# Optimization experiments

Hardware: AMD Instinct MI355X
Metric: run time of the kernel (lower is better)

The kernel has to match this reference:

```python
import jax, jax.numpy as jnp
import numpy as np

PAD_ID = 12975
HEADS = 16


def _sinusoid_table(n_position, d_hid):
    # pos / 10000^(2*(j//2)/d_hid), sin on even dims, cos on odd dims
    pos = jnp.arange(n_position, dtype=jnp.float32)[:, None]          # [P,1]
    j = jnp.arange(d_hid)
    angle = pos / jnp.power(10000.0, (2.0 * (j // 2) / d_hid).astype(jnp.float32))  # [P,D]
    table = jnp.where((j % 2) == 0, jnp.sin(angle), jnp.cos(angle))
    return table  # [P, D]


def setup_inputs() -> dict:
    key = jax.random.key(0)
    k1, k2 = jax.random.split(key)
    x = jax.random.randint(k1, (256, 200), 0, 32000, dtype=jnp.int64)
    weight = jax.random.normal(k2, (32000, 1024), dtype=jnp.float32) * 0.02
    return {"x": x, "weight": weight}


def reference(x, weight):
    B, S = x.shape
    D = weight.shape[1]

    # --- mask build (faithful to the python-loop semantics) ---
    m = x == PAD_ID                                   # [B,S]
    has_pad = jnp.any(m, axis=1)                      # [B]
    first = jnp.argmax(m, axis=1)                     # first True index (0 if none)
    # torch loop: if no True found, i ends at S-1 and idx[S-1:] is still set True
    first = jnp.where(has_pad, first, S - 1)          # [B]
    row_ge = jnp.arange(S)[None, :] >= first[:, None]  # [B,S] rows >= first are all-True
    remask = m[:, None, :] | row_ge[:, :, None]       # [B,S,S]
    mask = jnp.broadcast_to(remask[:, None, :, :], (B, HEADS, S, S))  # [B,H,S,S]

    # --- embedding + sinusoidal positional encoding (dropout in eval = identity) ---
    emb = weight[x]                                   # [B,S,D]
    pos_table = _sinusoid_table(S, D)                 # [S,D]
    out = emb + pos_table[None, :, :]                 # [B,S,D]
    return (out, mask)
```

## Files before the change

kernel.cpp:

```cpp
#include <hip/hip_runtime.h>
#include <math.h>

#define PAD_ID 12975
#define BB 256
#define SS 200
#define DD 1024
#define HH 16

#define WS_FIRST_BYTES 1024
#define WS_POST_BYTES  (SS * DD * 4)

__global__ void first_kernel(const int* __restrict__ x, int* __restrict__ first) {
    __shared__ int sfirst;
    const int b = blockIdx.x;
    if (threadIdx.x == 0) sfirst = SS - 1;
    __syncthreads();
    const int s = threadIdx.x;
    if (s < SS) {
        if (x[b * SS + s] == PAD_ID) atomicMin(&sfirst, s);
    }
    __syncthreads();
    if (threadIdx.x == 0) first[b] = sfirst;
}

__global__ void postable_kernel(float* __restrict__ posT) {
    const int idx = blockIdx.x * blockDim.x + threadIdx.x;
    if (idx >= SS * DD) return;
    const int s = idx >> 10;
    const int j = idx & (DD - 1);
    const int p = j >> 1;
    const float C = (float)(13.287712379549449 / 512.0);
    const float denom = exp2f((float)p * C);
    const float angle = (float)s / denom;
    posT[idx] = (j & 1) ? cosf(angle) : sinf(angle);
}

__global__ void mask_kernel(const int* __restrict__ x, const int* __restrict__ first,
                            float* __restrict__ mask) {
    const int total = BB * HH * SS * (SS / 4);
    const int stride = gridDim.x * blockDim.x;
    for (int c = blockIdx.x * blockDim.x + threadIdx.x; c < total; c += stride) {
        const int row = c / 50;
        const int j4  = c - row * 50;
        const int b   = row / (HH * SS);
        const int i   = row % SS;
        float4 v;
        if (i >= first[b]) {
            v = make_float4(1.f, 1.f, 1.f, 1.f);
        } else {
            const int4 xv = ((const int4*)x)[b * 50 + j4];
            v.x = (xv.x == PAD_ID) ? 1.f : 0.f;
            v.y = (xv.y == PAD_ID) ? 1.f : 0.f;
            v.z = (xv.z == PAD_ID) ? 1.f : 0.f;
            v.w = (xv.w == PAD_ID) ? 1.f : 0.f;
        }
        ((float4*)mask)[c] = v;
    }
}

__global__ void out_kernel(const int* __restrict__ x, const float* __restrict__ weight,
                           const float* __restrict__ posT, float* __restrict__ out) {
    const int row = blockIdx.x;
    const int s = row % SS;
    const int idx = x[row];
    const int t = threadIdx.x;
    const float4 w  = ((const float4*)(weight + (size_t)idx * DD))[t];
    const float4 pe = ((const float4*)(posT + (size_t)s * DD))[t];
    ((float4*)(out + (size_t)row * DD))[t] =
        make_float4(w.x + pe.x, w.y + pe.y, w.z + pe.z, w.w + pe.w);
}

__global__ void out_kernel_inline(const int* __restrict__ x, const float* __restrict__ weight,
                                  float* __restrict__ out) {
    const int row = blockIdx.x;
    const int s = row % SS;
    const int idx = x[row];
    const int t = threadIdx.x;
    const float C = (float)(13.287712379549449 / 512.0);
    const float p0 = (float)(2 * t);
    const float p1 = (float)(2 * t + 1);
    const float a0 = (float)s / exp2f(p0 * C);
    const float a1 = (float)s / exp2f(p1 * C);
    const float4 pe = make_float4(sinf(a0), cosf(a0), sinf(a1), cosf(a1));
    const float4 w = ((const float4*)(weight + (size_t)idx * DD))[t];
    ((float4*)(out + (size_t)row * DD))[t] =
        make_float4(w.x + pe.x, w.y + pe.y, w.z + pe.z, w.w + pe.w);
}

extern "C" void kernel_launch(void* const* d_in, const int* in_sizes, int n_in,
                              void* d_out, int out_size, void* d_ws, size_t ws_size,
                              hipStream_t stream) {
    const int*   x      = (const int*)d_in[0];
    const float* weight = (const float*)d_in[1];
    float* out  = (float*)d_out;
    float* mask = out + (size_t)BB * SS * DD;

    int*   first = (int*)d_ws;
    float* posT  = (float*)((char*)d_ws + WS_FIRST_BYTES);
    const bool useTable = ws_size >= (size_t)(WS_FIRST_BYTES + WS_POST_BYTES);

    first_kernel<<<BB, 256, 0, stream>>>(x, first);
    if (useTable) {
        postable_kernel<<<(SS * DD + 255) / 256, 256, 0, stream>>>(posT);
    }
    mask_kernel<<<8192, 256, 0, stream>>>(x, first, mask);
    if (useTable) {
        out_kernel<<<BB * SS, 256, 0, stream>>>(x, weight, posT, out);
    } else {
        out_kernel_inline<<<BB * SS, 256, 0, stream>>>(x, weight, out);
    }
}
```

Baseline: 193.3 us.

## Fuse prep and mask/output kernels into two launches with nontemporal stores

Merges the first-pad and positional-table kernels into one prep kernel, and runs the mask write and embedding+PE output in a single persistent kernel whose blocks are statically split between the two tasks. Both large write streams now use nontemporal stores. The aim is to cut launch overhead and let the two bandwidth-bound streams overlap. It drops the fallback for a small workspace, and the fixed block split may leave one half of the work finishing later than the other.

```diff
diff --git a/kernel.cpp b/kernel.cpp
--- a/kernel.cpp
+++ b/kernel.cpp
@@ -7,84 +7,75 @@
 #define DD 1024
 #define HH 16
 
+#define MASK_CHUNKS (BB * HH * SS * (SS / 4))
+#define OUT_ROWS    (BB * SS)
+
+#define NBLK 2048
+#define MBLK 1376
+
+typedef float f32x4 __attribute__((ext_vector_type(4)));
+typedef int   i32x4 __attribute__((ext_vector_type(4)));
+
 #define WS_FIRST_BYTES 1024
 #define WS_POST_BYTES  (SS * DD * 4)
 
-__global__ void first_kernel(const int* __restrict__ x, int* __restrict__ first) {
-    __shared__ int sfirst;
-    const int b = blockIdx.x;
-    if (threadIdx.x == 0) sfirst = SS - 1;
-    __syncthreads();
-    const int s = threadIdx.x;
-    if (s < SS) {
-        if (x[b * SS + s] == PAD_ID) atomicMin(&sfirst, s);
+__global__ void prep_kernel(const int* __restrict__ x, int* __restrict__ first,
+                            float* __restrict__ posT) {
+    const int idx = blockIdx.x * blockDim.x + threadIdx.x;
+    if (idx < SS * DD) {
+        const int s = idx >> 10;
+        const int j = idx & (DD - 1);
+        const int p = j >> 1;
+        const float C = (float)(13.287712379549449 / 512.0);
+        const float angle = (float)s / exp2f((float)p * C);
+        posT[idx] = (j & 1) ? cosf(angle) : sinf(angle);
     }
-    __syncthreads();
-    if (threadIdx.x == 0) first[b] = sfirst;
-}
-
-__global__ void postable_kernel(float* __restrict__ posT) {
-    const int idx = blockIdx.x * blockDim.x + threadIdx.x;
-    if (idx >= SS * DD) return;
-    const int s = idx >> 10;
-    const int j = idx & (DD - 1);
-    const int p = j >> 1;
-    const float C = (float)(13.287712379549449 / 512.0);
-    const float denom = exp2f((float)p * C);
-    const float angle = (float)s / denom;
-    posT[idx] = (j & 1) ? cosf(angle) : sinf(angle);
-}
-
-__global__ void mask_kernel(const int* __restrict__ x, const int* __restrict__ first,
-                            float* __restrict__ mask) {
-    const int total = BB * HH * SS * (SS / 4);
-    const int stride = gridDim.x * blockDim.x;
-    for (int c = blockIdx.x * blockDim.x + threadIdx.x; c < total; c += stride) {
-        const int row = c / 50;
-        const int j4  = c - row * 50;
-        const int b   = row / (HH * SS);
-        const int i   = row % SS;
-        float4 v;
-        if (i >= first[b]) {
-            v = make_float4(1.f, 1.f, 1.f, 1.f);
-        } else {
-            const int4 xv = ((const int4*)x)[b * 50 + j4];
-            v.x = (xv.x == PAD_ID) ? 1.f : 0.f;
-            v.y = (xv.y == PAD_ID) ? 1.f : 0.f;
-            v.z = (xv.z == PAD_ID) ? 1.f : 0.f;
-            v.w = (xv.w == PAD_ID) ? 1.f : 0.f;
-        }
-        ((float4*)mask)[c] = v;
+    if (blockIdx.x < BB) {
+        __shared__ int sfirst;
+        if (threadIdx.x == 0) sfirst = SS - 1;
+        __syncthreads();
+        if (threadIdx.x < SS && x[blockIdx.x * SS + threadIdx.x] == PAD_ID)
+            atomicMin(&sfirst, threadIdx.x);
+        __syncthreads();
+        if (threadIdx.x == 0) first[blockIdx.x] = sfirst;
     }
 }
 
-__global__ void out_kernel(const int* __restrict__ x, const float* __restrict__ weight,
-                           const float* __restrict__ posT, float* __restrict__ out) {
-    const int row = blockIdx.x;
-    const int s = row % SS;
-    const int idx = x[row];
-    const int t = threadIdx.x;
-    const float4 w  = ((const float4*)(weight + (size_t)idx * DD))[t];
-    const float4 pe = ((const float4*)(posT + (size_t)s * DD))[t];
-    ((float4*)(out + (size_t)row * DD))[t] =
-        make_float4(w.x + pe.x, w.y + pe.y, w.z + pe.z, w.w + pe.w);
-}
-
-__global__ void out_kernel_inline(const int* __restrict__ x, const float* __restrict__ weight,
-                                  float* __restrict__ out) {
-    const int row = blockIdx.x;
-    const int s = row % SS;
-    const int idx = x[row];
-    const int t = threadIdx.x;
-    const float C = (float)(13.287712379549449 / 512.0);
-    const float p0 = (float)(2 * t);
-    const float p1 = (float)(2 * t + 1);
-    const float a0 = (float)s / exp2f(p0 * C);
-    const float a1 = (float)s / exp2f(p1 * C);
-    const float4 pe = make_float4(sinf(a0), cosf(a0), sinf(a1), cosf(a1));
-    const float4 w = ((const float4*)(weight + (size_t)idx * DD))[t];
-    ((float4*)(out + (size_t)row * DD))[t] =
-        make_float4(w.x + pe.x, w.y + pe.y, w.z + pe.z, w.w + pe.w);
+__global__ void work_kernel(const int* __restrict__ x, const int* __restrict__ first,
+                            const float* __restrict__ weight, const float* __restrict__ posT,
+                            float* __restrict__ out, float* __restrict__ mask) {
+    if (blockIdx.x < MBLK) {
+        const int stride = MBLK * 256;
+        for (int c = blockIdx.x * 256 + threadIdx.x; c < MASK_CHUNKS; c += stride) {
+            const int row = c / 50;
+            const int j4  = c - row * 50;
+            const int b   = row / (HH * SS);
+            const int i   = row % SS;
+            f32x4 v;
+            if (i >= first[b]) {
+                v = (f32x4){1.f, 1.f, 1.f, 1.f};
+            } else {
+                const i32x4 xv = ((const i32x4*)x)[b * 50 + j4];
+                v.x = (xv.x == PAD_ID) ? 1.f : 0.f;
+                v.y = (xv.y == PAD_ID) ? 1.f : 0.f;
+                v.z = (xv.z == PAD_ID) ? 1.f : 0.f;
+                v.w = (xv.w == PAD_ID) ? 1.f : 0.f;
+            }
+            __builtin_nontemporal_store(v, (f32x4*)mask + c);
+        }
+    } else {
+        const int ob = blockIdx.x - MBLK;
+        const int OB = NBLK - MBLK;
+        for (int row = ob; row < OUT_ROWS; row += OB) {
+            const int s   = row % SS;
+            const int idx = x[row];
+            const int t   = threadIdx.x;
+            const f32x4 w  = ((const f32x4*)(weight + (size_t)idx * DD))[t];
+            const f32x4 pe = ((const f32x4*)(posT + (size_t)s * DD))[t];
+            const f32x4 r = w + pe;
+            __builtin_nontemporal_store(r, (f32x4*)(out + (size_t)row * DD) + t);
+        }
+    }
 }
 
 extern "C" void kernel_launch(void* const* d_in, const int* in_sizes, int n_in,
@@ -97,16 +88,7 @@
 
     int*   first = (int*)d_ws;
     float* posT  = (float*)((char*)d_ws + WS_FIRST_BYTES);
-    const bool useTable = ws_size >= (size_t)(WS_FIRST_BYTES + WS_POST_BYTES);
 
-    first_kernel<<<BB, 256, 0, stream>>>(x, first);
-    if (useTable) {
-        postable_kernel<<<(SS * DD + 255) / 256, 256, 0, stream>>>(posT);
-    }
-    mask_kernel<<<8192, 256, 0, stream>>>(x, first, mask);
-    if (useTable) {
-        out_kernel<<<BB * SS, 256, 0, stream>>>(x, weight, posT, out);
-    } else {
-        out_kernel_inline<<<BB * SS, 256, 0, stream>>>(x, weight, out);
-    }
+    prep_kernel<<<(SS * DD + 255) / 256, 256, 0, stream>>>(x, first, posT);
+    work_kernel<<<NBLK, 256, 0, stream>>>(x, first, weight, posT, out, mask);
 }
```

New measurement: 161.0 us. -16.7%, faster.
